# Kernel tuning notes

Measured on AMD Instinct MI355X. Metric: run time of the kernel, lower is better.

## Reference

```python
import jax, jax.numpy as jnp
import numpy as np

SHARPNESS = 2.0
EPS = 1e-12  # F.normalize default eps


def _l2norm_c(x):
    # L2-normalize along channel axis (axis=1), matching F.normalize(dim=1)
    n = jnp.sqrt(jnp.sum(x * x, axis=1, keepdims=True))
    return x / jnp.maximum(n, EPS)


def setup_inputs() -> dict:
    key = jax.random.key(0)
    k1, k2, k3 = jax.random.split(key, 3)
    N, C, H, W_ = 16, 256, 56, 56
    feat = jax.random.normal(k1, (N, C, H, W_), dtype=jnp.float32)
    W = jax.random.normal(k2, (C, C), dtype=jnp.float32) * 0.05  # 1x1 conv weight [out,in]
    b = jax.random.normal(k3, (C,), dtype=jnp.float32) * 0.05
    return {"feat": feat, "W": W, "b": b}


def reference(feat, W, b):
    N, C, H, W_ = feat.shape
    HW = H * W_
    # 1x1 conv == channel matmul
    feat_value = jnp.einsum('nchw,oc->nohw', feat, W) + b[None, :, None, None]
    feat_value = _l2norm_c(feat_value).reshape(N, C, HW)
    f = _l2norm_c(feat).reshape(N, C, HW)
    # correlation attention [N, HW, HW]
    attention = jnp.einsum('ncp,ncq->npq', f, f)
    attention = jnp.clip(attention, 0.0) ** SHARPNESS
    # bmm(feat_value, attention.transpose(1,2)) -> out[n,c,p] = sum_q fv[n,c,q] * att[n,p,q]
    out = jnp.einsum('ncq,npq->ncp', feat_value, attention)
    return out.reshape(N, C, H, W_)
```

## Files before the change

### kernel.cpp

```cpp
#include <hip/hip_runtime.h>

typedef unsigned short u16;
typedef unsigned int u32;
typedef __attribute__((ext_vector_type(8))) short short8;
typedef __attribute__((ext_vector_type(8))) u16 u16x8;
typedef __attribute__((ext_vector_type(4))) u32 u32x4;
typedef __attribute__((ext_vector_type(4))) float f32x4;

#define NB 16
#define CC 256
#define HW 3136
#define NT 49
#define NT2 98

__device__ __forceinline__ u16 f2bf(float x) {
  u32 u = __float_as_uint(x);
  u += 0x7fffu + ((u >> 16) & 1u);
  return (u16)(u >> 16);
}

__device__ __forceinline__ f32x4 mfma16(short8 a, short8 b, f32x4 c) {
  return __builtin_amdgcn_mfma_f32_16x16x32_bf16(a, b, c, 0, 0, 0);
}

__device__ __forceinline__ void gl_lds16(const void* g, void* l) {
  __builtin_amdgcn_global_load_lds(
      (const __attribute__((address_space(1))) void*)g,
      (__attribute__((address_space(3))) void*)l, 16, 0, 0);
}

__global__ __launch_bounds__(256) void k_cvtw(const float* __restrict__ W,
                                              u16* __restrict__ Wbf) {
  int i = (blockIdx.x * 256 + threadIdx.x) * 4;
  f32x4 v = *(const f32x4*)(W + i);
  u32 lo = (u32)f2bf(v[0]) | ((u32)f2bf(v[1]) << 16);
  u32 hi = (u32)f2bf(v[2]) | ((u32)f2bf(v[3]) << 16);
  *(u32*)(Wbf + i) = lo;
  *(u32*)(Wbf + i + 2) = hi;
}

__global__ __launch_bounds__(256) void k_prep_f(const float* __restrict__ feat,
                                                u16* __restrict__ f_bf,
                                                float* __restrict__ norm_f) {
  int pt = blockIdx.x, n = blockIdx.y;
  int tid = threadIdx.x;
  __shared__ float tile[256][65];
  __shared__ float rinv[64];
  const float* src = feat + (size_t)n * CC * HW + pt * 64;
  int p = tid & 63;
  #pragma unroll 8
  for (int c = tid >> 6; c < 256; c += 4)
    tile[c][p] = src[(size_t)c * HW + p];
  __syncthreads();
  if (tid < 64) {
    float s = 0.f;
    #pragma unroll 16
    for (int c = 0; c < 256; ++c) { float v = tile[c][tid]; s += v * v; }
    float nv = fmaxf(sqrtf(s), 1e-12f);
    rinv[tid] = 1.0f / nv;
    norm_f[n * HW + pt * 64 + tid] = nv;
  }
  __syncthreads();
  u16* dst = f_bf + ((size_t)n * HW + pt * 64) * 256;
  #pragma unroll
  for (int j = 0; j < 8; ++j) {
    int chunk = j * 256 + tid;
    int pp = chunk >> 5;
    int c0 = (chunk & 31) * 8;
    float inv = rinv[pp];
    u16x8 o;
    #pragma unroll
    for (int k = 0; k < 8; ++k) o[k] = f2bf(tile[c0 + k][pp] * inv);
    *(u16x8*)(dst + pp * 256 + c0) = o;
  }
}

__global__ __launch_bounds__(256) void k_conv(const u16* __restrict__ Wbf,
                                              const float* __restrict__ bias,
                                              const u16* __restrict__ f_bf,
                                              const float* __restrict__ norm_f,
                                              u16* __restrict__ fv_bf) {
  int qt = blockIdx.x, n = blockIdx.y;
  int tid = threadIdx.x;
  int lane = tid & 63, w = tid >> 6;
  int lr = lane & 15, lg = lane >> 4;
  __shared__ __align__(16) char fq[32768];
  __shared__ float wred[4][64];
  __shared__ float sinv[64];

  const char* fsrc = (const char*)(f_bf + ((size_t)n * HW + qt * 64) * 256);
  #pragma unroll
  for (int rep = 0; rep < 8; ++rep) {
    int linear = rep * 4096 + tid * 16;
    int q = linear >> 9;
    int cb = linear & 0x1F0;
    u32x4 v = *(const u32x4*)(fsrc + q * 512 + cb);
    *(u32x4*)(fq + q * 512 + (cb ^ ((q & 7) << 4))) = v;
  }
  __syncthreads();

  f32x4 acc[4][4] = {};
  #pragma unroll
  for (int kk = 0; kk < 8; ++kk) {
    short8 bfr[4], afr[4];
    #pragma unroll
    for (int j = 0; j < 4; ++j) {
      int q = j * 16 + lr;
      bfr[j] = *(const short8*)(fq + q * 512 + ((kk * 64 + lg * 16) ^ ((q & 7) << 4)));
    }
    #pragma unroll
    for (int i = 0; i < 4; ++i) {
      int o = w * 64 + i * 16 + lr;
      afr[i] = *(const short8*)((const char*)Wbf + (size_t)o * 512 + kk * 64 + lg * 16);
    }
    #pragma unroll
    for (int i = 0; i < 4; ++i)
      #pragma unroll
      for (int j = 0; j < 4; ++j)
        acc[i][j] = mfma16(afr[i], bfr[j], acc[i][j]);
  }

  float nf[4];
  #pragma unroll
  for (int j = 0; j < 4; ++j) nf[j] = norm_f[n * HW + qt * 64 + j * 16 + lr];
  float partial[4] = {0.f, 0.f, 0.f, 0.f};
  #pragma unroll
  for (int i = 0; i < 4; ++i)
    #pragma unroll
    for (int r = 0; r < 4; ++r) {
      float bv = bias[w * 64 + i * 16 + lg * 4 + r];
      #pragma unroll
      for (int j = 0; j < 4; ++j) {
        float pre = acc[i][j][r] * nf[j] + bv;
        acc[i][j][r] = pre;
        partial[j] += pre * pre;
      }
    }
  #pragma unroll
  for (int j = 0; j < 4; ++j) {
    float v = partial[j];
    v += __shfl_xor(v, 16);
    v += __shfl_xor(v, 32);
    if (lane < 16) wred[w][j * 16 + lane] = v;
  }
  __syncthreads();
  if (tid < 64) {
    float s = wred[0][tid] + wred[1][tid] + wred[2][tid] + wred[3][tid];
    sinv[tid] = 1.0f / fmaxf(sqrtf(s), 1e-12f);
  }
  __syncthreads();
  u16* dst = fv_bf + (size_t)n * CC * HW + qt * 64;
  #pragma unroll
  for (int i = 0; i < 4; ++i)
    #pragma unroll
    for (int r = 0; r < 4; ++r) {
      int o = w * 64 + i * 16 + lg * 4 + r;
      #pragma unroll
      for (int j = 0; j < 4; ++j) {
        int q = j * 16 + lr;
        dst[(size_t)o * HW + q] = f2bf(acc[i][j][r] * sinv[q]);
      }
    }
}

__global__ __launch_bounds__(256, 3) void k_attn(const u16* __restrict__ f_bf,
                                                 const u16* __restrict__ fv_bf,
                                                 float* __restrict__ out) {
  int linear = blockIdx.y * NT + blockIdx.x;
  int vb = (linear & 7) * 98 + (linear >> 3);
  int n = vb / NT;
  int pt = vb - n * NT;

  int tid = threadIdx.x;
  int lane = tid & 63, w = tid >> 6;
  int lr = lane & 15, lg = lane >> 4;
  __shared__ __align__(16) char fqd[2][16384];
  __shared__ __align__(16) char attl[5120];

  const char* fbase = (const char*)f_bf + (size_t)n * HW * 512;
  const char* fvbase = (const char*)fv_bf + (size_t)n * CC * HW * 2;

  int so[4];
  #pragma unroll
  for (int r = 0; r < 4; ++r) {
    int q = w * 8 + r * 2 + (lane >> 5);
    int col = (lane & 31) * 16;
    so[r] = q * 512 + (col ^ ((q & 7) << 4));
  }

  short8 ap[8];
  #pragma unroll
  for (int kk = 0; kk < 8; ++kk) {
    const char* pa = fbase + (size_t)(pt * 64 + w * 16 + lr) * 512 + kk * 64 + lg * 16;
    asm volatile("global_load_dwordx4 %0, %1, off"
                 : "=&v"(ap[kk]) : "v"(pa) : "memory");
  }
  asm volatile("s_waitcnt vmcnt(0)" ::: "memory");
  __builtin_amdgcn_sched_barrier(0);

  #pragma unroll
  for (int r = 0; r < 4; ++r)
    gl_lds16(fbase + so[r], (char*)fqd[0] + (w * 4 + r) * 1024);

  f32x4 oacc[4][4] = {};

  for (int qt = 0; qt < NT2; ++qt) {
    const char* fq = fqd[qt & 1];

    asm volatile("s_waitcnt vmcnt(0)" ::: "memory");
    __builtin_amdgcn_sched_barrier(0);
    __builtin_amdgcn_s_barrier();
    __builtin_amdgcn_sched_barrier(0);

    short8 av[4];
    #pragma unroll
    for (int fi = 0; fi < 4; ++fi) {
      const char* pa = fvbase + (size_t)(w * 64 + fi * 16 + lr) * (HW * 2)
                       + qt * 64 + lg * 16;
      asm volatile("global_load_dwordx4 %0, %1, off"
                   : "=&v"(av[fi]) : "v"(pa) : "memory");
    }

    if (qt + 1 < NT2) {
      const char* fsrc = fbase + (size_t)(qt + 1) * 16384;
      char* dbuf = (char*)fqd[(qt + 1) & 1];
      #pragma unroll
      for (int r = 0; r < 4; ++r)
        gl_lds16(fsrc + so[r], dbuf + (w * 4 + r) * 1024);
    }

    f32x4 s[2] = {};
    #pragma unroll
    for (int kk = 0; kk < 8; ++kk) {
      short8 bq[2];
      #pragma unroll
      for (int fj = 0; fj < 2; ++fj) {
        int q = fj * 16 + lr;
        bq[fj] = *(const short8*)(fq + q * 512 + ((kk * 64 + lg * 16) ^ ((q & 7) << 4)));
      }
      s[0] = mfma16(ap[kk], bq[0], s[0]);
      s[1] = mfma16(ap[kk], bq[1], s[1]);
    }

    #pragma unroll
    for (int fj = 0; fj < 2; ++fj)
      #pragma unroll
      for (int r = 0; r < 4; ++r) {
        float v = s[fj][r];
        v = fmaxf(v, 0.f);
        v = v * v;
        int p = w * 16 + lg * 4 + r;
        int q = fj * 16 + lr;
        *(u16*)(attl + p * 80 + q * 2) = f2bf(v);
      }
    asm volatile("s_waitcnt lgkmcnt(0)" ::: "memory");
    __builtin_amdgcn_sched_barrier(0);
    __builtin_amdgcn_s_barrier();
    __builtin_amdgcn_sched_barrier(0);

    if (qt + 1 < NT2) {
      asm volatile("s_waitcnt vmcnt(4)" ::: "memory");
    } else {
      asm volatile("s_waitcnt vmcnt(0)" ::: "memory");
    }
    __builtin_amdgcn_sched_barrier(0);

    short8 bt[4];
    #pragma unroll
    for (int fp = 0; fp < 4; ++fp)
      bt[fp] = *(const short8*)(attl + (fp * 16 + lr) * 80 + lg * 16);
    #pragma unroll
    for (int fi = 0; fi < 4; ++fi)
      #pragma unroll
      for (int fp = 0; fp < 4; ++fp)
        oacc[fi][fp] = mfma16(av[fi], bt[fp], oacc[fi][fp]);
  }

  float* op = out + (size_t)n * CC * HW + pt * 64;
  #pragma unroll
  for (int fi = 0; fi < 4; ++fi)
    #pragma unroll
    for (int r = 0; r < 4; ++r) {
      int c = w * 64 + fi * 16 + lg * 4 + r;
      #pragma unroll
      for (int fp = 0; fp < 4; ++fp)
        op[(size_t)c * HW + fp * 16 + lr] = oacc[fi][fp][r];
    }
}

extern "C" void kernel_launch(void* const* d_in, const int* in_sizes, int n_in,
                              void* d_out, int out_size, void* d_ws, size_t ws_size,
                              hipStream_t stream) {
  const float* feat = (const float*)d_in[0];
  const float* W    = (const float*)d_in[1];
  const float* bias = (const float*)d_in[2];
  float* out = (float*)d_out;

  char* ws = (char*)d_ws;
  u16*   Wbf    = (u16*)ws;
  float* norm_f = (float*)(ws + 131072);
  u16*   f_bf   = (u16*)(ws + 331776);
  u16*   fv_bf  = (u16*)(ws + 26021888);

  k_cvtw<<<dim3(64), dim3(256), 0, stream>>>(W, Wbf);
  k_prep_f<<<dim3(NT, NB), dim3(256), 0, stream>>>(feat, f_bf, norm_f);
  k_conv<<<dim3(NT, NB), dim3(256), 0, stream>>>(Wbf, bias, f_bf, norm_f, fv_bf);
  k_attn<<<dim3(NT, NB), dim3(256), 0, stream>>>(f_bf, fv_bf, out);
}
```

Before: 362.5 us.

## Keep attention tile in registers via lane shuffles, each wave owning 16 pixels across all channels

Restructures k_attn so each wave computes the transposed score tile for its own 16 pixels and rearranges the squared bf16 scores into an MFMA B operand with cross-lane shuffles. This removes the LDS attention buffer and the second block-wide barrier per iteration. Each wave now loads all 256 channel rows of fv directly from global memory (16 loads per iteration, up from 4), which raises per-wave global traffic and relies on cache hits. Occupancy is raised to 4 blocks per SM, and the prefetch is moved after compute with inline-asm waits replaced by plain loads.

```diff
diff --git a/kernel.cpp b/kernel.cpp
--- a/kernel.cpp
+++ b/kernel.cpp
@@ -17,6 +17,10 @@
   u32 u = __float_as_uint(x);
   u += 0x7fffu + ((u >> 16) & 1u);
   return (u16)(u >> 16);
+}
+
+__device__ __forceinline__ u32 pk2(float a, float b) {
+  return (u32)f2bf(a) | ((u32)f2bf(b) << 16);
 }
 
 __device__ __forceinline__ f32x4 mfma16(short8 a, short8 b, f32x4 c) {
@@ -163,7 +167,7 @@
     }
 }
 
-__global__ __launch_bounds__(256, 3) void k_attn(const u16* __restrict__ f_bf,
+__global__ __launch_bounds__(256, 4) void k_attn(const u16* __restrict__ f_bf,
                                                  const u16* __restrict__ fv_bf,
                                                  float* __restrict__ out) {
   int linear = blockIdx.y * NT + blockIdx.x;
@@ -175,7 +179,6 @@
   int lane = tid & 63, w = tid >> 6;
   int lr = lane & 15, lg = lane >> 4;
   __shared__ __align__(16) char fqd[2][16384];
-  __shared__ __align__(16) char attl[5120];
 
   const char* fbase = (const char*)f_bf + (size_t)n * HW * 512;
   const char* fvbase = (const char*)fv_bf + (size_t)n * CC * HW * 2;
@@ -190,19 +193,15 @@
 
   short8 ap[8];
   #pragma unroll
-  for (int kk = 0; kk < 8; ++kk) {
-    const char* pa = fbase + (size_t)(pt * 64 + w * 16 + lr) * 512 + kk * 64 + lg * 16;
-    asm volatile("global_load_dwordx4 %0, %1, off"
-                 : "=&v"(ap[kk]) : "v"(pa) : "memory");
-  }
-  asm volatile("s_waitcnt vmcnt(0)" ::: "memory");
-  __builtin_amdgcn_sched_barrier(0);
+  for (int kk = 0; kk < 8; ++kk)
+    ap[kk] = *(const short8*)(fbase + (size_t)(pt * 64 + w * 16 + lr) * 512 +
+                              kk * 64 + lg * 16);
 
   #pragma unroll
   for (int r = 0; r < 4; ++r)
     gl_lds16(fbase + so[r], (char*)fqd[0] + (w * 4 + r) * 1024);
 
-  f32x4 oacc[4][4] = {};
+  f32x4 oacc[16] = {};
 
   for (int qt = 0; qt < NT2; ++qt) {
     const char* fq = fqd[qt & 1];
@@ -212,15 +211,48 @@
     __builtin_amdgcn_s_barrier();
     __builtin_amdgcn_sched_barrier(0);
 
-    short8 av[4];
-    #pragma unroll
-    for (int fi = 0; fi < 4; ++fi) {
-      const char* pa = fvbase + (size_t)(w * 64 + fi * 16 + lr) * (HW * 2)
-                       + qt * 64 + lg * 16;
-      asm volatile("global_load_dwordx4 %0, %1, off"
-                   : "=&v"(av[fi]) : "v"(pa) : "memory");
-    }
-
+    f32x4 s0 = {0.f, 0.f, 0.f, 0.f}, s1 = {0.f, 0.f, 0.f, 0.f};
+    #pragma unroll
+    for (int kk = 0; kk < 8; ++kk) {
+      int q0 = lr, q1 = 16 + lr;
+      short8 aq0 = *(const short8*)(fq + q0 * 512 +
+                                    ((kk * 64 + lg * 16) ^ ((q0 & 7) << 4)));
+      short8 aq1 = *(const short8*)(fq + q1 * 512 +
+                                    ((kk * 64 + lg * 16) ^ ((q1 & 7) << 4)));
+      s0 = mfma16(aq0, ap[kk], s0);
+      s1 = mfma16(aq1, ap[kk], s1);
+    }
+
+    f32x4 e0, e1;
+    #pragma unroll
+    for (int r = 0; r < 4; ++r) {
+      float v0 = fmaxf(s0[r], 0.f); e0[r] = v0 * v0;
+      float v1 = fmaxf(s1[r], 0.f); e1[r] = v1 * v1;
+    }
+    u32 c00 = pk2(e0[0], e0[1]), c01 = pk2(e0[2], e0[3]);
+    u32 c10 = pk2(e1[0], e1[1]), c11 = pk2(e1[2], e1[3]);
+    int srcA = (lg & 1) * 32 + lr;
+    int srcB = srcA + 16;
+    u32 t0a = __shfl(c00, srcA), t1a = __shfl(c10, srcA);
+    u32 t0b = __shfl(c01, srcA), t1b = __shfl(c11, srcA);
+    u32 u0a = __shfl(c00, srcB), u1a = __shfl(c10, srcB);
+    u32 u0b = __shfl(c01, srcB), u1b = __shfl(c11, srcB);
+    bool hi = lg >= 2;
+    u32x4 bw;
+    bw[0] = hi ? t1a : t0a;
+    bw[1] = hi ? t1b : t0b;
+    bw[2] = hi ? u1a : u0a;
+    bw[3] = hi ? u1b : u0b;
+    short8 bt = __builtin_bit_cast(short8, bw);
+
+    #pragma unroll
+    for (int cf = 0; cf < 16; ++cf) {
+      short8 av = *(const short8*)(fvbase + (size_t)(cf * 16 + lr) * (HW * 2) +
+                                   qt * 64 + lg * 16);
+      oacc[cf] = mfma16(av, bt, oacc[cf]);
+    }
+
+    __builtin_amdgcn_sched_barrier(0);
     if (qt + 1 < NT2) {
       const char* fsrc = fbase + (size_t)(qt + 1) * 16384;
       char* dbuf = (char*)fqd[(qt + 1) & 1];
@@ -228,64 +260,15 @@
       for (int r = 0; r < 4; ++r)
         gl_lds16(fsrc + so[r], dbuf + (w * 4 + r) * 1024);
     }
-
-    f32x4 s[2] = {};
-    #pragma unroll
-    for (int kk = 0; kk < 8; ++kk) {
-      short8 bq[2];
-      #pragma unroll
-      for (int fj = 0; fj < 2; ++fj) {
-        int q = fj * 16 + lr;
-        bq[fj] = *(const short8*)(fq + q * 512 + ((kk * 64 + lg * 16) ^ ((q & 7) << 4)));
-      }
-      s[0] = mfma16(ap[kk], bq[0], s[0]);
-      s[1] = mfma16(ap[kk], bq[1], s[1]);
-    }
-
-    #pragma unroll
-    for (int fj = 0; fj < 2; ++fj)
-      #pragma unroll
-      for (int r = 0; r < 4; ++r) {
-        float v = s[fj][r];
-        v = fmaxf(v, 0.f);
-        v = v * v;
-        int p = w * 16 + lg * 4 + r;
-        int q = fj * 16 + lr;
-        *(u16*)(attl + p * 80 + q * 2) = f2bf(v);
-      }
-    asm volatile("s_waitcnt lgkmcnt(0)" ::: "memory");
-    __builtin_amdgcn_sched_barrier(0);
-    __builtin_amdgcn_s_barrier();
-    __builtin_amdgcn_sched_barrier(0);
-
-    if (qt + 1 < NT2) {
-      asm volatile("s_waitcnt vmcnt(4)" ::: "memory");
-    } else {
-      asm volatile("s_waitcnt vmcnt(0)" ::: "memory");
-    }
-    __builtin_amdgcn_sched_barrier(0);
-
-    short8 bt[4];
-    #pragma unroll
-    for (int fp = 0; fp < 4; ++fp)
-      bt[fp] = *(const short8*)(attl + (fp * 16 + lr) * 80 + lg * 16);
-    #pragma unroll
-    for (int fi = 0; fi < 4; ++fi)
-      #pragma unroll
-      for (int fp = 0; fp < 4; ++fp)
-        oacc[fi][fp] = mfma16(av[fi], bt[fp], oacc[fi][fp]);
-  }
-
-  float* op = out + (size_t)n * CC * HW + pt * 64;
-  #pragma unroll
-  for (int fi = 0; fi < 4; ++fi)
-    #pragma unroll
-    for (int r = 0; r < 4; ++r) {
-      int c = w * 64 + fi * 16 + lg * 4 + r;
-      #pragma unroll
-      for (int fp = 0; fp < 4; ++fp)
-        op[(size_t)c * HW + fp * 16 + lr] = oacc[fi][fp][r];
-    }
+    __builtin_amdgcn_sched_barrier(0);
+  }
+
+  float* op = out + (size_t)n * CC * HW + pt * 64 + w * 16 + lr;
+  #pragma unroll
+  for (int cf = 0; cf < 16; ++cf)
+    #pragma unroll
+    for (int r = 0; r < 4; ++r)
+      op[(size_t)(cf * 16 + lg * 4 + r) * HW] = oacc[cf][r];
 }
 
 extern "C" void kernel_launch(void* const* d_in, const int* in_sizes, int n_in,
```

Measured after the change: 860.3 us. +137.3%, slower.

## Widen attention q-tile to 64 with 8-wave blocks splitting p/q and c/p

Applied to the files above, without the earlier changes.

The attention kernel now runs 512-thread blocks and processes 64 keys per iteration instead of 32, halving the loop trip count and the number of barriers. Each wave covers a 16x32 p/q quadrant for the score product and a 64x32 c/p quadrant for the output product, with an XOR-swizzled LDS attention tile. Hand-written asm global loads become plain loads, so the compiler now places its own waits. In exchange, the double-buffered key tile and attention tile double LDS use, which may limit how many blocks fit per CU.

```diff
diff --git a/kernel.cpp b/kernel.cpp
--- a/kernel.cpp
+++ b/kernel.cpp
@@ -11,12 +11,16 @@
 #define CC 256
 #define HW 3136
 #define NT 49
-#define NT2 98
 
 __device__ __forceinline__ u16 f2bf(float x) {
   u32 u = __float_as_uint(x);
   u += 0x7fffu + ((u >> 16) & 1u);
   return (u16)(u >> 16);
+}
+
+__device__ __forceinline__ float relu2(float v) {
+  v = fmaxf(v, 0.f);
+  return v * v;
 }
 
 __device__ __forceinline__ f32x4 mfma16(short8 a, short8 b, f32x4 c) {
@@ -163,7 +167,7 @@
     }
 }
 
-__global__ __launch_bounds__(256, 3) void k_attn(const u16* __restrict__ f_bf,
+__global__ __launch_bounds__(512, 4) void k_attn(const u16* __restrict__ f_bf,
                                                  const u16* __restrict__ fv_bf,
                                                  float* __restrict__ out) {
   int linear = blockIdx.y * NT + blockIdx.x;
@@ -174,8 +178,10 @@
   int tid = threadIdx.x;
   int lane = tid & 63, w = tid >> 6;
   int lr = lane & 15, lg = lane >> 4;
-  __shared__ __align__(16) char fqd[2][16384];
-  __shared__ __align__(16) char attl[5120];
+  int wp1 = w & 3, wq1 = w >> 2;
+  int wc = w & 3, wp2 = w >> 2;
+  __shared__ __align__(16) char fqd[2][32768];
+  __shared__ __align__(16) char attl[8192];
 
   const char* fbase = (const char*)f_bf + (size_t)n * HW * 512;
   const char* fvbase = (const char*)fv_bf + (size_t)n * CC * HW * 2;
@@ -183,28 +189,24 @@
   int so[4];
   #pragma unroll
   for (int r = 0; r < 4; ++r) {
-    int q = w * 8 + r * 2 + (lane >> 5);
+    int q = (w * 4 + r) * 2 + (lane >> 5);
     int col = (lane & 31) * 16;
     so[r] = q * 512 + (col ^ ((q & 7) << 4));
   }
 
   short8 ap[8];
   #pragma unroll
-  for (int kk = 0; kk < 8; ++kk) {
-    const char* pa = fbase + (size_t)(pt * 64 + w * 16 + lr) * 512 + kk * 64 + lg * 16;
-    asm volatile("global_load_dwordx4 %0, %1, off"
-                 : "=&v"(ap[kk]) : "v"(pa) : "memory");
-  }
-  asm volatile("s_waitcnt vmcnt(0)" ::: "memory");
-  __builtin_amdgcn_sched_barrier(0);
+  for (int kk = 0; kk < 8; ++kk)
+    ap[kk] = *(const short8*)(fbase + (size_t)(pt * 64 + wp1 * 16 + lr) * 512 +
+                              kk * 64 + lg * 16);
 
   #pragma unroll
   for (int r = 0; r < 4; ++r)
     gl_lds16(fbase + so[r], (char*)fqd[0] + (w * 4 + r) * 1024);
 
-  f32x4 oacc[4][4] = {};
-
-  for (int qt = 0; qt < NT2; ++qt) {
+  f32x4 oacc[4][2] = {};
+
+  for (int qt = 0; qt < NT; ++qt) {
     const char* fq = fqd[qt & 1];
 
     asm volatile("s_waitcnt vmcnt(0)" ::: "memory");
@@ -212,17 +214,17 @@
     __builtin_amdgcn_s_barrier();
     __builtin_amdgcn_sched_barrier(0);
 
-    short8 av[4];
-    #pragma unroll
-    for (int fi = 0; fi < 4; ++fi) {
-      const char* pa = fvbase + (size_t)(w * 64 + fi * 16 + lr) * (HW * 2)
-                       + qt * 64 + lg * 16;
-      asm volatile("global_load_dwordx4 %0, %1, off"
-                   : "=&v"(av[fi]) : "v"(pa) : "memory");
-    }
-
-    if (qt + 1 < NT2) {
-      const char* fsrc = fbase + (size_t)(qt + 1) * 16384;
+    short8 av[2][4];
+    #pragma unroll
+    for (int kk = 0; kk < 2; ++kk)
+      #pragma unroll
+      for (int fi = 0; fi < 4; ++fi)
+        av[kk][fi] = *(const short8*)(fvbase +
+                        (size_t)(wc * 64 + fi * 16 + lr) * (HW * 2) +
+                        qt * 128 + kk * 64 + lg * 16);
+
+    if (qt + 1 < NT) {
+      const char* fsrc = fbase + (size_t)(qt + 1) * 32768;
       char* dbuf = (char*)fqd[(qt + 1) & 1];
       #pragma unroll
       for (int r = 0; r < 4; ++r)
@@ -232,59 +234,61 @@
     f32x4 s[2] = {};
     #pragma unroll
     for (int kk = 0; kk < 8; ++kk) {
-      short8 bq[2];
       #pragma unroll
       for (int fj = 0; fj < 2; ++fj) {
-        int q = fj * 16 + lr;
-        bq[fj] = *(const short8*)(fq + q * 512 + ((kk * 64 + lg * 16) ^ ((q & 7) << 4)));
-      }
-      s[0] = mfma16(ap[kk], bq[0], s[0]);
-      s[1] = mfma16(ap[kk], bq[1], s[1]);
+        int q = wq1 * 32 + fj * 16 + lr;
+        short8 bq = *(const short8*)(fq + q * 512 +
+                                     ((kk * 64 + lg * 16) ^ ((q & 7) << 4)));
+        s[fj] = mfma16(ap[kk], bq, s[fj]);
+      }
     }
 
     #pragma unroll
     for (int fj = 0; fj < 2; ++fj)
       #pragma unroll
       for (int r = 0; r < 4; ++r) {
-        float v = s[fj][r];
-        v = fmaxf(v, 0.f);
-        v = v * v;
-        int p = w * 16 + lg * 4 + r;
-        int q = fj * 16 + lr;
-        *(u16*)(attl + p * 80 + q * 2) = f2bf(v);
+        int p = wp1 * 16 + lg * 4 + r;
+        int q = wq1 * 32 + fj * 16 + lr;
+        *(u16*)(attl + p * 128 + ((q * 2) ^ ((p & 7) << 4))) = f2bf(relu2(s[fj][r]));
       }
     asm volatile("s_waitcnt lgkmcnt(0)" ::: "memory");
     __builtin_amdgcn_sched_barrier(0);
     __builtin_amdgcn_s_barrier();
     __builtin_amdgcn_sched_barrier(0);
 
-    if (qt + 1 < NT2) {
+    if (qt + 1 < NT) {
       asm volatile("s_waitcnt vmcnt(4)" ::: "memory");
     } else {
       asm volatile("s_waitcnt vmcnt(0)" ::: "memory");
     }
     __builtin_amdgcn_sched_barrier(0);
 
-    short8 bt[4];
-    #pragma unroll
-    for (int fp = 0; fp < 4; ++fp)
-      bt[fp] = *(const short8*)(attl + (fp * 16 + lr) * 80 + lg * 16);
-    #pragma unroll
-    for (int fi = 0; fi < 4; ++fi)
-      #pragma unroll
-      for (int fp = 0; fp < 4; ++fp)
-        oacc[fi][fp] = mfma16(av[fi], bt[fp], oacc[fi][fp]);
-  }
-
-  float* op = out + (size_t)n * CC * HW + pt * 64;
+    #pragma unroll
+    for (int kk = 0; kk < 2; ++kk) {
+      short8 bt[2];
+      #pragma unroll
+      for (int fp = 0; fp < 2; ++fp) {
+        int p = wp2 * 32 + fp * 16 + lr;
+        bt[fp] = *(const short8*)(attl + p * 128 +
+                                  ((kk * 64 + lg * 16) ^ ((p & 7) << 4)));
+      }
+      #pragma unroll
+      for (int fi = 0; fi < 4; ++fi)
+        #pragma unroll
+        for (int fp = 0; fp < 2; ++fp)
+          oacc[fi][fp] = mfma16(av[kk][fi], bt[fp], oacc[fi][fp]);
+    }
+  }
+
+  float* op = out + (size_t)n * CC * HW + pt * 64 + wp2 * 32 + lr;
   #pragma unroll
   for (int fi = 0; fi < 4; ++fi)
     #pragma unroll
     for (int r = 0; r < 4; ++r) {
-      int c = w * 64 + fi * 16 + lg * 4 + r;
-      #pragma unroll
-      for (int fp = 0; fp < 4; ++fp)
-        op[(size_t)c * HW + fp * 16 + lr] = oacc[fi][fp][r];
+      int c = wc * 64 + fi * 16 + lg * 4 + r;
+      #pragma unroll
+      for (int fp = 0; fp < 2; ++fp)
+        op[(size_t)c * HW + fp * 16] = oacc[fi][fp][r];
     }
 }
 
@@ -305,5 +309,5 @@
   k_cvtw<<<dim3(64), dim3(256), 0, stream>>>(W, Wbf);
   k_prep_f<<<dim3(NT, NB), dim3(256), 0, stream>>>(feat, f_bf, norm_f);
   k_conv<<<dim3(NT, NB), dim3(256), 0, stream>>>(Wbf, bias, f_bf, norm_f, fv_bf);
-  k_attn<<<dim3(NT, NB), dim3(256), 0, stream>>>(f_bf, fv_bf, out);
-}
+  k_attn<<<dim3(NT, NB), dim3(512), 0, stream>>>(f_bf, fv_bf, out);
+}
```

New measurement: 622.2 us. +71.6%, slower.
